# Kernel tuning notes

Hardware: AMD Instinct MI355X
Metric: run time of the kernel (lower is better)

Reference implementation:

```python
import jax, jax.numpy as jnp
import numpy as np

N = 100000       # num_nodes
E = 1600000      # num edges
C = 1000         # num_communities
NE = 128         # n_embedding
NID = 64         # n_id_embedding
NH = 128         # n_hidden


def setup_inputs() -> dict:
    key = jax.random.key(0)
    ks = jax.random.split(key, 24)
    s = 0.05  # small init scale for weights
    inp = {
        "x": jax.random.normal(ks[0], (N, 19), dtype=jnp.float32),
        "edge_index": jax.random.randint(ks[1], (2, E), 0, N, dtype=jnp.int64),
        "community": jax.random.randint(ks[2], (N,), 0, C, dtype=jnp.int64),
        "id_embeddings": jax.random.normal(ks[3], (N, NID), dtype=jnp.float32),
        "W_emb1": jax.random.normal(ks[4], (7, NE), dtype=jnp.float32) * s,
        "b_emb1": jnp.zeros((NE,), jnp.float32),
        "W_emb2": jax.random.normal(ks[5], (12, NE), dtype=jnp.float32) * s,
        "b_emb2": jnp.zeros((NE,), jnp.float32),
        "W_emb3": jax.random.normal(ks[6], (2 * NE + NID, 2 * NE + NID), dtype=jnp.float32) * s,
        "b_emb3": jnp.zeros((2 * NE + NID,), jnp.float32),
        "W_conv1": jax.random.normal(ks[7], (2 * NE + NID, NH), dtype=jnp.float32) * s,
        "b_conv1": jnp.zeros((NH,), jnp.float32),
        "W_conv2": jax.random.normal(ks[8], (NH, NH), dtype=jnp.float32) * s,
        "b_conv2": jnp.zeros((NH,), jnp.float32),
        "W_lin1": jax.random.normal(ks[9], (2 * NH, NH), dtype=jnp.float32) * s,
        "b_lin1": jnp.zeros((NH,), jnp.float32),
        "W_lin2": jax.random.normal(ks[10], (NH, 1), dtype=jnp.float32) * s,
        "b_lin2": jnp.zeros((1,), jnp.float32),
    }
    return inp


def _gcn_conv(h, W, b, src, dst, deg_inv_sqrt):
    # PyG GCNConv: D^{-1/2}(A+I)D^{-1/2} (h W) + b, self-loops included.
    hw = h @ W                                   # [N, out]
    norm = deg_inv_sqrt[src] * deg_inv_sqrt[dst]  # [E]
    msg = hw[src] * norm[:, None]                # [E, out] gather
    agg = jax.ops.segment_sum(msg, dst, num_segments=N)
    agg = agg + hw * (deg_inv_sqrt ** 2)[:, None]  # self-loop term (norm = 1/deg)
    return agg + b


def _community_pool(h, community):
    # scatter_mean over community ids, then cat([mean, mean], dim=1)
    sums = jax.ops.segment_sum(h, community, num_segments=C)
    cnt = jax.ops.segment_sum(jnp.ones((h.shape[0],), h.dtype), community, num_segments=C)
    mean = sums / jnp.maximum(cnt, 1.0)[:, None]
    return jnp.concatenate([mean, mean], axis=1)


def reference(x, edge_index, community, id_embeddings,
              W_emb1, b_emb1, W_emb2, b_emb2, W_emb3, b_emb3,
              W_conv1, b_conv1, W_conv2, b_conv2,
              W_lin1, b_lin1, W_lin2, b_lin2):
    src, dst = edge_index[0], edge_index[1]
    # degree (with self-loops) on dst, as in PyG gcn_norm
    deg = jax.ops.segment_sum(jnp.ones((E,), jnp.float32), dst, num_segments=N) + 1.0
    deg_inv_sqrt = deg ** -0.5

    x1 = jax.nn.relu(x[:, :7] @ W_emb1 + b_emb1)
    x2 = jax.nn.relu(x[:, 7:] @ W_emb2 + b_emb2)
    h = jnp.concatenate([x1, x2, id_embeddings], axis=1)   # [N, 320]
    h = jax.nn.relu(h @ W_emb3 + b_emb3)

    h = jax.nn.relu(_gcn_conv(h, W_conv1, b_conv1, src, dst, deg_inv_sqrt))
    p1 = _community_pool(h, community)                      # [C, 2*NH]
    h = jax.nn.relu(_gcn_conv(h, W_conv2, b_conv2, src, dst, deg_inv_sqrt))
    p2 = _community_pool(h, community)                      # [C, 2*NH]

    z = p1 + p2
    z = jax.nn.relu(z @ W_lin1 + b_lin1)
    # dropout is identity in eval mode (training=False)
    out = (z @ W_lin2 + b_lin2).squeeze(-1)                 # [C]
    return out
```

## Files before the change

### kernel.cpp

```cpp
#include <hip/hip_runtime.h>
#include <hip/hip_bf16.h>
#include <cstddef>

#define NN 100000
#define EE 1600000
#define CC 1000
#define NBK ((NN + 255) / 256)
#define EPB 4096

#define FP8_SCALE 32.0f
#define FP8_INV   0.03125f

using short8 = __attribute__((ext_vector_type(8))) short;
using f32x4  = __attribute__((ext_vector_type(4))) float;
using f32x2  = __attribute__((ext_vector_type(2))) float;

__device__ __forceinline__ float bf2f(unsigned int u) {
    union { unsigned int i; float f; } x; x.i = u << 16; return x.f;
}
__device__ __forceinline__ unsigned short f2bf(float f) {
    __hip_bfloat16 h = __float2bfloat16(f);
    return *reinterpret_cast<unsigned short*>(&h);
}
__device__ __forceinline__ unsigned int pack2(float lo, float hi) {
    return ((unsigned int)f2bf(hi) << 16) | f2bf(lo);
}
__device__ __forceinline__ unsigned char f2fp8(float v) {
    unsigned int p = __builtin_amdgcn_cvt_pk_fp8_f32(v, v, 0, false);
    return (unsigned char)(p & 0xffu);
}
__device__ __forceinline__ f32x2 fp8x2f(unsigned int u16) {
    return __builtin_amdgcn_cvt_pk_f32_fp8(u16, false);
}

__global__ void k_init(int* __restrict__ bucketCnt, int* __restrict__ bucketFill,
                       int* __restrict__ commcnt) {
    int i = blockIdx.x * 256 + threadIdx.x;
    if (i < NBK) { bucketCnt[i] = 0; bucketFill[i] = 0; }
    if (i < CC) commcnt[i] = 0;
}

__global__ __launch_bounds__(256) void k_bhist(const int* __restrict__ dst,
                                               int* __restrict__ bucketCnt) {
    __shared__ int hist[NBK];
    int t = threadIdx.x;
    for (int i = t; i < NBK; i += 256) hist[i] = 0;
    __syncthreads();
    int base = blockIdx.x * EPB;
    for (int i = t; i < EPB; i += 256) {
        int e = base + i;
        if (e < EE) atomicAdd(&hist[dst[e] >> 8], 1);
    }
    __syncthreads();
    for (int i = t; i < NBK; i += 256)
        if (hist[i]) atomicAdd(&bucketCnt[i], hist[i]);
}

__global__ void k_bscan(const int* __restrict__ bucketCnt, int* __restrict__ bucketBase) {
    __shared__ int sd[512];
    int t = threadIdx.x;
    int v = (t < NBK) ? bucketCnt[t] : 0;
    sd[t] = v;
    __syncthreads();
    for (int off = 1; off < 512; off <<= 1) {
        int x = (t >= off) ? sd[t - off] : 0;
        __syncthreads();
        sd[t] += x;
        __syncthreads();
    }
    if (t < NBK) bucketBase[t] = sd[t] - v;
    if (t == 0) bucketBase[NBK] = EE;
}

__global__ __launch_bounds__(256) void k_bucketize(
    const int* __restrict__ src, const int* __restrict__ dst,
    const int* __restrict__ bucketBase, int* __restrict__ bucketFill,
    int2* __restrict__ bkt) {
    __shared__ int hist[NBK];
    __shared__ int runPos[NBK];
    int t = threadIdx.x;
    for (int i = t; i < NBK; i += 256) hist[i] = 0;
    __syncthreads();
    int base = blockIdx.x * EPB;
    for (int i = t; i < EPB; i += 256) {
        int e = base + i;
        if (e < EE) atomicAdd(&hist[dst[e] >> 8], 1);
    }
    __syncthreads();
    for (int i = t; i < NBK; i += 256)
        runPos[i] = hist[i] ? (bucketBase[i] + atomicAdd(&bucketFill[i], hist[i])) : 0;
    __syncthreads();
    for (int i = t; i < EPB; i += 256) {
        int e = base + i;
        if (e < EE) {
            int d = dst[e];
            int pos = atomicAdd(&runPos[d >> 8], 1);
            bkt[pos] = make_int2(src[e], d);
        }
    }
}

__global__ __launch_bounds__(256) void k_csr(
    const int2* __restrict__ bkt, const int* __restrict__ bucketBase,
    const int* __restrict__ comm, int* __restrict__ commcnt,
    int* __restrict__ rowofs, float* __restrict__ dis, int* __restrict__ csr) {
    __shared__ int cnt[256], sd[256], cnt2[256];
    int b = blockIdx.x, t = threadIdx.x;
    int base = bucketBase[b], end = bucketBase[b + 1];
    int nodeBase = b << 8;
    cnt[t] = 0; cnt2[t] = 0;
    __syncthreads();
    for (int i = base + t; i < end; i += 256)
        atomicAdd(&cnt[bkt[i].y - nodeBase], 1);
    __syncthreads();
    int v = cnt[t];
    sd[t] = v;
    __syncthreads();
    for (int off = 1; off < 256; off <<= 1) {
        int x = (t >= off) ? sd[t - off] : 0;
        __syncthreads();
        sd[t] += x;
        __syncthreads();
    }
    int ofs = sd[t] - v;
    sd[t] = ofs;
    int node = nodeBase + t;
    if (node < NN) {
        rowofs[node] = base + ofs;
        dis[node] = rsqrtf((float)v + 1.0f);
        atomicAdd(&commcnt[comm[node]], 1);
    }
    if (b == NBK - 1 && t == 0) rowofs[NN] = EE;
    __syncthreads();
    for (int i = base + t; i < end; i += 256) {
        int2 ed = bkt[i];
        int ld = ed.y - nodeBase;
        int p = atomicAdd(&cnt2[ld], 1);
        csr[base + sd[ld] + p] = ed.x;
    }
}

__global__ void k_scanc(int* __restrict__ commcnt, int* __restrict__ commofs) {
    __shared__ int sd[1024];
    int t = threadIdx.x;
    int v = (t < CC) ? commcnt[t] : 0;
    sd[t] = v;
    __syncthreads();
    for (int off = 1; off < 1024; off <<= 1) {
        int x = (t >= off) ? sd[t - off] : 0;
        __syncthreads();
        sd[t] += x;
        __syncthreads();
    }
    if (t < CC) {
        commofs[t] = sd[t] - v;
        commcnt[t] = 0;
    }
    if (t == CC - 1) commofs[CC] = sd[t];
}

__global__ void k_fillc(const int* __restrict__ comm, const int* __restrict__ commofs,
                        int* __restrict__ commcnt, int* __restrict__ members) {
    int i = blockIdx.x * 256 + threadIdx.x;
    if (i >= NN) return;
    int c = comm[i];
    int pos = commofs[c] + atomicAdd(&commcnt[c], 1);
    members[pos] = i;
}

__global__ void k_wconv(const float* __restrict__ W3, unsigned short* __restrict__ W3t,
                        const float* __restrict__ Wc1, unsigned short* __restrict__ Wc1t,
                        const float* __restrict__ Wc2, unsigned short* __restrict__ Wc2t) {
    int y = blockIdx.y;
    int k = blockIdx.x * 256 + threadIdx.x;
    if (y < 320) {
        if (k < 328) W3t[(size_t)y * 328 + k] = (k < 320) ? f2bf(W3[(size_t)k * 320 + y]) : 0;
    } else if (y < 448) {
        int n = y - 320;
        if (k < 328) Wc1t[(size_t)n * 328 + k] = (k < 320) ? f2bf(Wc1[(size_t)k * 128 + n]) : 0;
    } else {
        int n = y - 448;
        if (k < 136) Wc2t[(size_t)n * 136 + k] = (k < 128) ? f2bf(Wc2[(size_t)k * 128 + n]) : 0;
    }
}

__global__ __launch_bounds__(256) void k_embed(
    const float* __restrict__ x, const float* __restrict__ id_emb,
    const float* __restrict__ W1, const float* __restrict__ b1,
    const float* __restrict__ W2, const float* __restrict__ b2,
    unsigned short* __restrict__ h0) {
    __shared__ float W1s[7][128];
    __shared__ float W2s[12][128];
    __shared__ float b1s[128], b2s[128];
    __shared__ float xs[64][20];
    int t = threadIdx.x;
    int base = blockIdx.x * 64;
    for (int i = t; i < 7 * 128; i += 256) ((float*)W1s)[i] = W1[i];
    for (int i = t; i < 12 * 128; i += 256) ((float*)W2s)[i] = W2[i];
    if (t < 128) { b1s[t] = b1[t]; b2s[t] = b2[t]; }
    for (int i = t; i < 64 * 19; i += 256) {
        int r = i / 19, cc = i % 19;
        int node = base + r;
        xs[r][cc] = (node < NN) ? x[(size_t)node * 19 + cc] : 0.f;
    }
    __syncthreads();
    int ln = t >> 6, lane = t & 63;
    int c2 = lane * 2;
    for (int nn = ln; nn < 64; nn += 4) {
        int node = base + nn;
        if (node >= NN) break;
        unsigned int* orow = (unsigned int*)(h0 + (size_t)node * 320);
        float a0 = b1s[c2], a1 = b1s[c2 + 1];
        #pragma unroll
        for (int k = 0; k < 7; ++k) {
            float xv = xs[nn][k];
            float2 w = *(const float2*)&W1s[k][c2];
            a0 += xv * w.x; a1 += xv * w.y;
        }
        orow[lane] = pack2(fmaxf(a0, 0.f), fmaxf(a1, 0.f));
        a0 = b2s[c2]; a1 = b2s[c2 + 1];
        #pragma unroll
        for (int k = 0; k < 12; ++k) {
            float xv = xs[nn][7 + k];
            float2 w = *(const float2*)&W2s[k][c2];
            a0 += xv * w.x; a1 += xv * w.y;
        }
        orow[64 + lane] = pack2(fmaxf(a0, 0.f), fmaxf(a1, 0.f));
        if (lane < 32) {
            float2 iv = *(const float2*)(id_emb + (size_t)node * 64 + c2);
            orow[128 + lane] = pack2(iv.x, iv.y);
        }
    }
}

template <int K, int N, int RELU, int OUT8>
__global__ __launch_bounds__(256) void k_bgemm(
    const unsigned short* __restrict__ A, const unsigned short* __restrict__ Bt,
    const float* __restrict__ bias, void* __restrict__ Cv, int M) {
    constexpr int NT = (N + 127) / 128;
    __shared__ __align__(16) short sbuf[2 * 128 * 40];
    short (*As)[40] = (short(*)[40])sbuf;
    short (*Bs)[40] = (short(*)[40])(sbuf + 128 * 40);
    int t = threadIdx.x;
    int bid = blockIdx.x;
    int ct = bid % NT, rblk = bid / NT;
    int rowBase = rblk * 128, colBase = ct * 128;
    int wid = t >> 6, lane = t & 63;
    int wm = wid >> 1, wn = wid & 1;
    int fr = lane & 15, g = lane >> 4;
    int rr = t >> 2;
    int qq = (t & 3) * 8;
    f32x4 acc[4][4] = {};
    short8 z = {};
    short8 pA0, pA1, pB0, pB1;
    int grA0 = rowBase + rr, grA1 = grA0 + 64;
    int gcB0 = colBase + rr, gcB1 = gcB0 + 64;
    pA0 = (grA0 < M) ? *(const short8*)(A + (size_t)grA0 * K + qq) : z;
    pA1 = (grA1 < M) ? *(const short8*)(A + (size_t)grA1 * K + qq) : z;
    pB0 = (gcB0 < N) ? *(const short8*)(Bt + (size_t)gcB0 * (K + 8) + qq) : z;
    pB1 = (gcB1 < N) ? *(const short8*)(Bt + (size_t)gcB1 * (K + 8) + qq) : z;
    for (int kb = 0; kb < K; kb += 32) {
        __syncthreads();
        *(short8*)&As[rr][qq]      = pA0;
        *(short8*)&As[rr + 64][qq] = pA1;
        *(short8*)&Bs[rr][qq]      = pB0;
        *(short8*)&Bs[rr + 64][qq] = pB1;
        __syncthreads();
        if (kb + 32 < K) {
            int kn = kb + 32;
            pA0 = (grA0 < M) ? *(const short8*)(A + (size_t)grA0 * K + kn + qq) : z;
            pA1 = (grA1 < M) ? *(const short8*)(A + (size_t)grA1 * K + kn + qq) : z;
            pB0 = (gcB0 < N) ? *(const short8*)(Bt + (size_t)gcB0 * (K + 8) + kn + qq) : z;
            pB1 = (gcB1 < N) ? *(const short8*)(Bt + (size_t)gcB1 * (K + 8) + kn + qq) : z;
        }
        short8 bfr[4];
        #pragma unroll
        for (int nf = 0; nf < 4; ++nf)
            bfr[nf] = *(const short8*)&Bs[wn * 64 + nf * 16 + fr][g * 8];
        #pragma unroll
        for (int mf = 0; mf < 4; ++mf) {
            short8 a = *(const short8*)&As[wm * 64 + mf * 16 + fr][g * 8];
            #pragma unroll
            for (int nf = 0; nf < 4; ++nf)
                acc[mf][nf] = __builtin_amdgcn_mfma_f32_16x16x32_bf16(a, bfr[nf], acc[mf][nf], 0, 0, 0);
        }
    }
    if (!OUT8) {
        unsigned short* sb = (unsigned short*)sbuf;
        #pragma unroll
        for (int cc = 0; cc < 2; ++cc) {
            int cbase = colBase + cc * 64;
            if (cbase < N) {
                __syncthreads();
                if (wn == cc) {
                    #pragma unroll
                    for (int nf = 0; nf < 4; ++nf) {
                        int colL = nf * 16 + fr;
                        float bv = RELU ? bias[cbase + colL] : 0.f;
                        #pragma unroll
                        for (int mf = 0; mf < 4; ++mf) {
                            #pragma unroll
                            for (int r = 0; r < 4; ++r) {
                                int row = wm * 64 + mf * 16 + g * 4 + r;
                                float v = acc[mf][nf][r];
                                if (RELU) v = fmaxf(v + bv, 0.f);
                                sb[row * 64 + colL] = f2bf(v);
                            }
                        }
                    }
                }
                __syncthreads();
                #pragma unroll
                for (int i = 0; i < 4; ++i) {
                    int off8 = t + 256 * i;
                    int row = off8 >> 3;
                    int col = (off8 & 7) * 8;
                    int grow = rowBase + row;
                    if (grow < M)
                        *(short8*)((unsigned short*)Cv + (size_t)grow * N + cbase + col) =
                            *(const short8*)&sb[row * 64 + col];
                }
            }
        }
    } else {
        unsigned char* sb8 = (unsigned char*)sbuf;
        __syncthreads();
        #pragma unroll
        for (int nf = 0; nf < 4; ++nf) {
            int colL = wn * 64 + nf * 16 + fr;
            #pragma unroll
            for (int mf = 0; mf < 4; ++mf) {
                #pragma unroll
                for (int r = 0; r < 4; ++r) {
                    int row = wm * 64 + mf * 16 + g * 4 + r;
                    sb8[row * 128 + colL] = f2fp8(acc[mf][nf][r] * FP8_SCALE);
                }
            }
        }
        __syncthreads();
        #pragma unroll
        for (int i = 0; i < 4; ++i) {
            int off16 = t + 256 * i;
            int row = off16 >> 3;
            int col = (off16 & 7) * 16;
            int grow = rowBase + row;
            if (grow < M)
                *(int4*)((unsigned char*)Cv + (size_t)grow * N + col) =
                    *(const int4*)&sb8[row * 128 + col];
        }
    }
}

__global__ __launch_bounds__(256) void k_gather(
    const int* __restrict__ rowofs, const int* __restrict__ csr,
    const float* __restrict__ dis, const unsigned char* __restrict__ hw8,
    const float* __restrict__ bias, unsigned short* __restrict__ hout) {
    int wid = blockIdx.x * 4 + (threadIdx.x >> 6);
    wid = __builtin_amdgcn_readfirstlane(wid);
    int lane = threadIdx.x & 63;
    if (wid >= NN) return;
    int ro = rowofs[wid], re = rowofs[wid + 1];
    int c = lane * 2;
    float dsd = dis[wid];
    unsigned int hv = *(const unsigned short*)(hw8 + (size_t)wid * 128 + c);
    f32x2 hf = fp8x2f(hv);
    float a0 = hf.x * dsd;
    float a1 = hf.y * dsd;
    int e = ro;
    for (; e + 16 <= re; e += 16) {
        int s[16]; float n[16]; unsigned int v[16];
        #pragma unroll
        for (int j = 0; j < 16; ++j) s[j] = csr[e + j];
        #pragma unroll
        for (int j = 0; j < 16; ++j) n[j] = dis[s[j]];
        #pragma unroll
        for (int j = 0; j < 16; ++j)
            v[j] = *(const unsigned short*)(hw8 + (size_t)s[j] * 128 + c);
        #pragma unroll
        for (int j = 0; j < 16; ++j) {
            f32x2 f = fp8x2f(v[j]);
            a0 += f.x * n[j];
            a1 += f.y * n[j];
        }
    }
    for (; e + 4 <= re; e += 4) {
        int s[4]; float n[4]; unsigned int v[4];
        #pragma unroll
        for (int j = 0; j < 4; ++j) s[j] = csr[e + j];
        #pragma unroll
        for (int j = 0; j < 4; ++j) n[j] = dis[s[j]];
        #pragma unroll
        for (int j = 0; j < 4; ++j)
            v[j] = *(const unsigned short*)(hw8 + (size_t)s[j] * 128 + c);
        #pragma unroll
        for (int j = 0; j < 4; ++j) {
            f32x2 f = fp8x2f(v[j]);
            a0 += f.x * n[j];
            a1 += f.y * n[j];
        }
    }
    for (; e < re; ++e) {
        int s0 = csr[e];
        float n0 = dis[s0];
        unsigned int v0 = *(const unsigned short*)(hw8 + (size_t)s0 * 128 + c);
        f32x2 f = fp8x2f(v0);
        a0 += f.x * n0;
        a1 += f.y * n0;
    }
    a0 = fmaxf(a0 * dsd * FP8_INV + bias[c], 0.f);
    a1 = fmaxf(a1 * dsd * FP8_INV + bias[c + 1], 0.f);
    *(unsigned int*)(hout + (size_t)wid * 128 + c) = pack2(a0, a1);
}

__global__ __launch_bounds__(128) void k_final(
    const unsigned short* __restrict__ h2, const unsigned short* __restrict__ h3,
    const int* __restrict__ commofs, const int* __restrict__ members,
    const float* __restrict__ Wl1, const float* __restrict__ bl1,
    const float* __restrict__ Wl2, const float* __restrict__ bl2,
    float* __restrict__ out) {
    __shared__ float zh[128];
    __shared__ float partial[2];
    int c = blockIdx.x, t = threadIdx.x;
    int ro = commofs[c], re = commofs[c + 1];
    float acc = 0.f;
    int e = ro;
    for (; e + 4 <= re; e += 4) {
        int m0 = members[e], m1 = members[e + 1];
        int m2 = members[e + 2], m3 = members[e + 3];
        acc += bf2f(h2[(size_t)m0 * 128 + t]) + bf2f(h3[(size_t)m0 * 128 + t]);
        acc += bf2f(h2[(size_t)m1 * 128 + t]) + bf2f(h3[(size_t)m1 * 128 + t]);
        acc += bf2f(h2[(size_t)m2 * 128 + t]) + bf2f(h3[(size_t)m2 * 128 + t]);
        acc += bf2f(h2[(size_t)m3 * 128 + t]) + bf2f(h3[(size_t)m3 * 128 + t]);
    }
    for (; e < re; ++e) {
        int m = members[e];
        acc += bf2f(h2[(size_t)m * 128 + t]) + bf2f(h3[(size_t)m * 128 + t]);
    }
    float invc = 1.0f / fmaxf((float)(re - ro), 1.0f);
    zh[t] = acc * invc;
    __syncthreads();
    float a = bl1[t];
    for (int k = 0; k < 128; ++k)
        a += zh[k] * (Wl1[(size_t)k * 128 + t] + Wl1[(size_t)(k + 128) * 128 + t]);
    float zv = fmaxf(a, 0.f);
    float p = zv * Wl2[t];
    #pragma unroll
    for (int off = 32; off > 0; off >>= 1) p += __shfl_down(p, off, 64);
    if ((t & 63) == 0) partial[t >> 6] = p;
    __syncthreads();
    if (t == 0) out[c] = partial[0] + partial[1] + bl2[0];
}

extern "C" void kernel_launch(void* const* d_in, const int* in_sizes, int n_in,
                              void* d_out, int out_size, void* d_ws, size_t ws_size,
                              hipStream_t stream) {
    const float* x       = (const float*)d_in[0];
    const int*   edge    = (const int*)d_in[1];
    const int*   comm    = (const int*)d_in[2];
    const float* id_emb  = (const float*)d_in[3];
    const float* W1      = (const float*)d_in[4];
    const float* b1      = (const float*)d_in[5];
    const float* W2      = (const float*)d_in[6];
    const float* b2      = (const float*)d_in[7];
    const float* W3      = (const float*)d_in[8];
    const float* b3      = (const float*)d_in[9];
    const float* Wc1     = (const float*)d_in[10];
    const float* bc1     = (const float*)d_in[11];
    const float* Wc2     = (const float*)d_in[12];
    const float* bc2     = (const float*)d_in[13];
    const float* Wl1     = (const float*)d_in[14];
    const float* bl1     = (const float*)d_in[15];
    const float* Wl2     = (const float*)d_in[16];
    const float* bl2     = (const float*)d_in[17];
    float* out = (float*)d_out;
    float* ws  = (float*)d_ws;

    const int* srcIdx = edge;
    const int* dstIdx = edge + EE;

    size_t o = 0;
    auto alloc = [&](size_t nfloats) {
        float* p = ws + o; o += (nfloats + 3) & ~(size_t)3; return p;
    };
    float* dis      = alloc(NN);
    int* rowofs     = (int*)alloc(NN + 8);
    int* bucketCnt  = (int*)alloc(NBK + 8);
    int* bucketBase = (int*)alloc(NBK + 8);
    int* bucketFill = (int*)alloc(NBK + 8);
    int* commcnt    = (int*)alloc(1024);
    int* commofs    = (int*)alloc(1024 + 8);
    int* members    = (int*)alloc(NN);
    int2* bkt       = (int2*)alloc((size_t)EE * 2);
    int* csr        = (int*)alloc(EE);
    unsigned short* W3t  = (unsigned short*)alloc(320 * 328 / 2);
    unsigned short* Wc1t = (unsigned short*)alloc(128 * 328 / 2);
    unsigned short* Wc2t = (unsigned short*)alloc(128 * 136 / 2);
    unsigned short* h0   = (unsigned short*)alloc((size_t)NN * 320 / 2);
    unsigned short* h1   = (unsigned short*)alloc((size_t)NN * 320 / 2);
    unsigned char*  hw8  = (unsigned char*)alloc((size_t)NN * 128 / 4);
    unsigned short* h2   = (unsigned short*)alloc((size_t)NN * 128 / 2);
    unsigned short* h3   = (unsigned short*)alloc((size_t)NN * 128 / 2);

    k_init<<<4, 256, 0, stream>>>(bucketCnt, bucketFill, commcnt);
    k_bhist<<<NBK, 256, 0, stream>>>(dstIdx, bucketCnt);
    k_bscan<<<1, 512, 0, stream>>>(bucketCnt, bucketBase);
    k_bucketize<<<NBK, 256, 0, stream>>>(srcIdx, dstIdx, bucketBase, bucketFill, bkt);
    k_csr<<<NBK, 256, 0, stream>>>(bkt, bucketBase, comm, commcnt, rowofs, dis, csr);
    k_scanc<<<1, 1024, 0, stream>>>(commcnt, commofs);
    k_fillc<<<NBK, 256, 0, stream>>>(comm, commofs, commcnt, members);

    k_wconv<<<dim3(2, 576), 256, 0, stream>>>(W3, W3t, Wc1, Wc1t, Wc2, Wc2t);

    k_embed<<<(NN + 63) / 64, 256, 0, stream>>>(x, id_emb, W1, b1, W2, b2, h0);

    int rb = (NN + 127) / 128;
    k_bgemm<320, 320, 1, 0><<<rb * 3, 256, 0, stream>>>(h0, W3t, b3, h1, NN);
    k_bgemm<320, 128, 0, 1><<<rb, 256, 0, stream>>>(h1, Wc1t, nullptr, hw8, NN);
    k_gather<<<(NN + 3) / 4, 256, 0, stream>>>(rowofs, csr, dis, hw8, bc1, h2);
    k_bgemm<128, 128, 0, 1><<<rb, 256, 0, stream>>>(h2, Wc2t, nullptr, hw8, NN);
    k_gather<<<(NN + 3) / 4, 256, 0, stream>>>(rowofs, csr, dis, hw8, bc2, h3);

    k_final<<<CC, 128, 0, stream>>>(h2, h3, commofs, members, Wl1, bl1, Wl2, bl2, out);
}
```

Measured before the change: 378.9 us.

## Double-buffer LDS tiles in bf16 GEMM, remap blocks per XCD, pad epilogue stride

Converts the GEMM main loop from a single LDS buffer with two barriers per k-step to ping-pong buffers with one barrier per step. The next tile is written to the alternate buffer after the MFMAs. When there are multiple column tiles, block IDs are remapped so consecutive tiles land on the same XCD, which is meant to improve L2 reuse of A rows. The bf16 epilogue staging stride is padded from 64 to 72 to reduce LDS bank conflicts. The cost is double the LDS footprint, which may lower occupancy.

```diff
diff --git a/kernel.cpp b/kernel.cpp
--- a/kernel.cpp
+++ b/kernel.cpp
@@ -238,11 +238,15 @@
     const unsigned short* __restrict__ A, const unsigned short* __restrict__ Bt,
     const float* __restrict__ bias, void* __restrict__ Cv, int M) {
     constexpr int NT = (N + 127) / 128;
-    __shared__ __align__(16) short sbuf[2 * 128 * 40];
-    short (*As)[40] = (short(*)[40])sbuf;
-    short (*Bs)[40] = (short(*)[40])(sbuf + 128 * 40);
+    __shared__ __align__(16) short sbuf[2][10240];
     int t = threadIdx.x;
     int bid = blockIdx.x;
+    if constexpr (NT > 1) {
+        int nwg = gridDim.x;
+        int q = nwg >> 3, r = nwg & 7;
+        int xcd = bid & 7, idx = bid >> 3;
+        bid = (xcd < r ? xcd * (q + 1) : r * (q + 1) + (xcd - r) * q) + idx;
+    }
     int ct = bid % NT, rblk = bid / NT;
     int rowBase = rblk * 128, colBase = ct * 128;
     int wid = t >> 6, lane = t & 63;
@@ -259,39 +263,56 @@
     pA1 = (grA1 < M) ? *(const short8*)(A + (size_t)grA1 * K + qq) : z;
     pB0 = (gcB0 < N) ? *(const short8*)(Bt + (size_t)gcB0 * (K + 8) + qq) : z;
     pB1 = (gcB1 < N) ? *(const short8*)(Bt + (size_t)gcB1 * (K + 8) + qq) : z;
+    {
+        short* As = sbuf[0];
+        short* Bs = sbuf[0] + 128 * 40;
+        *(short8*)&As[rr * 40 + qq]        = pA0;
+        *(short8*)&As[(rr + 64) * 40 + qq] = pA1;
+        *(short8*)&Bs[rr * 40 + qq]        = pB0;
+        *(short8*)&Bs[(rr + 64) * 40 + qq] = pB1;
+    }
+    __syncthreads();
+    int cur = 0;
     for (int kb = 0; kb < K; kb += 32) {
-        __syncthreads();
-        *(short8*)&As[rr][qq]      = pA0;
-        *(short8*)&As[rr + 64][qq] = pA1;
-        *(short8*)&Bs[rr][qq]      = pB0;
-        *(short8*)&Bs[rr + 64][qq] = pB1;
-        __syncthreads();
-        if (kb + 32 < K) {
+        bool more = (kb + 32 < K);
+        if (more) {
             int kn = kb + 32;
             pA0 = (grA0 < M) ? *(const short8*)(A + (size_t)grA0 * K + kn + qq) : z;
             pA1 = (grA1 < M) ? *(const short8*)(A + (size_t)grA1 * K + kn + qq) : z;
             pB0 = (gcB0 < N) ? *(const short8*)(Bt + (size_t)gcB0 * (K + 8) + kn + qq) : z;
             pB1 = (gcB1 < N) ? *(const short8*)(Bt + (size_t)gcB1 * (K + 8) + kn + qq) : z;
         }
+        const short* As = sbuf[cur];
+        const short* Bs = sbuf[cur] + 128 * 40;
         short8 bfr[4];
         #pragma unroll
         for (int nf = 0; nf < 4; ++nf)
-            bfr[nf] = *(const short8*)&Bs[wn * 64 + nf * 16 + fr][g * 8];
+            bfr[nf] = *(const short8*)&Bs[(wn * 64 + nf * 16 + fr) * 40 + g * 8];
         #pragma unroll
         for (int mf = 0; mf < 4; ++mf) {
-            short8 a = *(const short8*)&As[wm * 64 + mf * 16 + fr][g * 8];
+            short8 a = *(const short8*)&As[(wm * 64 + mf * 16 + fr) * 40 + g * 8];
             #pragma unroll
             for (int nf = 0; nf < 4; ++nf)
                 acc[mf][nf] = __builtin_amdgcn_mfma_f32_16x16x32_bf16(a, bfr[nf], acc[mf][nf], 0, 0, 0);
         }
+        if (more) {
+            short* Asn = sbuf[cur ^ 1];
+            short* Bsn = sbuf[cur ^ 1] + 128 * 40;
+            *(short8*)&Asn[rr * 40 + qq]        = pA0;
+            *(short8*)&Asn[(rr + 64) * 40 + qq] = pA1;
+            *(short8*)&Bsn[rr * 40 + qq]        = pB0;
+            *(short8*)&Bsn[(rr + 64) * 40 + qq] = pB1;
+        }
+        __syncthreads();
+        cur ^= 1;
     }
     if (!OUT8) {
-        unsigned short* sb = (unsigned short*)sbuf;
+        unsigned short* sb = (unsigned short*)sbuf[0];
         #pragma unroll
         for (int cc = 0; cc < 2; ++cc) {
             int cbase = colBase + cc * 64;
             if (cbase < N) {
-                __syncthreads();
+                if (cc) __syncthreads();
                 if (wn == cc) {
                     #pragma unroll
                     for (int nf = 0; nf < 4; ++nf) {
@@ -304,7 +325,7 @@
                                 int row = wm * 64 + mf * 16 + g * 4 + r;
                                 float v = acc[mf][nf][r];
                                 if (RELU) v = fmaxf(v + bv, 0.f);
-                                sb[row * 64 + colL] = f2bf(v);
+                                sb[row * 72 + colL] = f2bf(v);
                             }
                         }
                     }
@@ -318,13 +339,12 @@
                     int grow = rowBase + row;
                     if (grow < M)
                         *(short8*)((unsigned short*)Cv + (size_t)grow * N + cbase + col) =
-                            *(const short8*)&sb[row * 64 + col];
+                            *(const short8*)&sb[row * 72 + col];
                 }
             }
         }
     } else {
-        unsigned char* sb8 = (unsigned char*)sbuf;
-        __syncthreads();
+        unsigned char* sb8 = (unsigned char*)sbuf[0];
         #pragma unroll
         for (int nf = 0; nf < 4; ++nf) {
             int colL = wn * 64 + nf * 16 + fr;
```

Result: no change. 380.8 us (+0.5%).
